# Optimization experiments

Hardware: AMD Instinct MI355X
Metric: run time of the kernel (lower is better)

## Reference

```python
import jax, jax.numpy as jnp
import numpy as np

T = 16384   # sequence length (timesteps)
E = 1024    # embedding_size
H = 1024    # h_size == vocab (logits are the raw LSTM hidden output)


def setup_inputs() -> dict:
    key = jax.random.key(0)
    ks = jax.random.split(key, 6)
    s = 1.0 / np.sqrt(H)  # torch LSTM default init: U(-1/sqrt(H), 1/sqrt(H))
    Xs = jax.random.normal(ks[0], (T, E), jnp.float32)
    W_ih = jax.random.uniform(ks[1], (4 * H, E), jnp.float32, -s, s)
    W_hh = jax.random.uniform(ks[2], (4 * H, H), jnp.float32, -s, s)
    b_ih = jax.random.uniform(ks[3], (4 * H,), jnp.float32, -s, s)
    b_hh = jax.random.uniform(ks[4], (4 * H,), jnp.float32, -s, s)
    ys = jax.random.randint(ks[5], (T,), 0, H, dtype=jnp.int64)
    return {"Xs": Xs, "W_ih": W_ih, "W_hh": W_hh, "b_ih": b_ih, "b_hh": b_hh, "ys": ys}


def reference(Xs, W_ih, W_hh, b_ih, b_hh, ys):
    h_size = W_hh.shape[1]
    # input projections for all timesteps in one GEMM: [T, 4H]
    xg = Xs @ W_ih.T + b_ih + b_hh

    def step(carry, inp):
        h, c = carry
        xg_t, y_t = inp
        gates = xg_t + W_hh @ h  # [4H], torch gate order i,f,g,o
        i = jax.nn.sigmoid(gates[0 * h_size:1 * h_size])
        f = jax.nn.sigmoid(gates[1 * h_size:2 * h_size])
        g = jnp.tanh(gates[2 * h_size:3 * h_size])
        o = jax.nn.sigmoid(gates[3 * h_size:4 * h_size])
        c = f * c + i * g
        h = o * jnp.tanh(c)
        # cross-entropy on raw hidden output (vocab == h_size), batch 1
        loss_t = jax.nn.logsumexp(h) - h[y_t]
        return (h, c), loss_t

    h0 = jnp.zeros((h_size,), Xs.dtype)
    c0 = jnp.zeros((h_size,), Xs.dtype)
    (_, _), losses = jax.lax.scan(step, (h0, c0), (xg, ys))
    return jnp.sum(losses)
```

## Files before the change

kernel.cpp:

```cpp
#include <hip/hip_runtime.h>
#include <hip/hip_cooperative_groups.h>
#include <cstddef>

namespace cg = cooperative_groups;

#define T_STEPS 16384
#define E_DIM   1024
#define H_DIM   1024
#define G4      4096

#define NWG 128
#define NTH 512
#define EPW 8
#define CH  512
#define NCHUNK (T_STEPS / CH)
#define TKc 32

#define LDA(p)    __hip_atomic_load((p), __ATOMIC_RELAXED, __HIP_MEMORY_SCOPE_AGENT)
#define STA(p, v) __hip_atomic_store((p), (v), __ATOMIC_RELAXED, __HIP_MEMORY_SCOPE_AGENT)


__global__ __launch_bounds__(NTH) void lstm_fused_kernel(
    const float* __restrict__ Xs, const float* __restrict__ Wih,
    const float* __restrict__ Whh, const float* __restrict__ bih,
    const float* __restrict__ bhh, const int* __restrict__ ys,
    float* __restrict__ xgc,
    unsigned long long* __restrict__ hslot,
    float* __restrict__ partials,
    float* __restrict__ hy,
    float* __restrict__ wsum,
    float* __restrict__ out)
{
    cg::grid_group grid = cg::this_grid();
    const int w    = blockIdx.x;
    const int tid  = threadIdx.x;
    const int lane = tid & 63;
    const int j    = tid >> 6;
    const int gj   = w * EPW + j;

    __shared__ float hs[2][H_DIM];
    __shared__ float ered[16][EPW];
    __shared__ float red[8];
    __shared__ float As[TKc][68];
    __shared__ float Bs[TKc][132];

    float Wreg[4][16];
#pragma unroll
    for (int g = 0; g < 4; ++g) {
        const float* wr = Whh + (size_t)(g * H_DIM + gj) * H_DIM + lane;
#pragma unroll
        for (int m = 0; m < 16; ++m) Wreg[g][m] = wr[m << 6];
    }

    float c_state = 0.f;
    if (lane == 0) STA(&hslot[gj], 1ull << 32);

    const int nt   = w & 31;
    const int n0   = nt * 128;
    const int tx4  = (tid & 31) * 4;
    const int ty4  = (tid >> 5) * 4;
    const int lrow = tid >> 3;
    const int lkg  = (tid & 7) * 4;

    float4 bias_v;
    {
        const float4 bi = *(const float4*)&bih[n0 + tx4];
        const float4 bh = *(const float4*)&bhh[n0 + tx4];
        bias_v.x = bi.x + bh.x; bias_v.y = bi.y + bh.y;
        bias_v.z = bi.z + bh.z; bias_v.w = bi.w + bh.w;
    }

    const float gate_scale = (lane == 2) ? 2.f : 1.f;
    const float gate_mul   = (lane == 2) ? 2.f : 1.f;
    const float gate_add   = (lane == 2) ? -1.f : 0.f;

    float xv = 0.f;
    int   yt = 0;

    for (int c = 0; c < NCHUNK; ++c) {
        const int t0 = c * CH;

#pragma unroll
        for (int rep = 0; rep < 2; ++rep) {
            const int mt = (w >> 5) + rep * 4;
            float acc[4][4];
#pragma unroll
            for (int i = 0; i < 4; ++i)
#pragma unroll
                for (int jj = 0; jj < 4; ++jj) acc[i][jj] = 0.f;

            const float* Arow = Xs + (size_t)(t0 + mt * 64 + lrow) * E_DIM + lkg;

            for (int kc = 0; kc < E_DIM; kc += TKc) {
                __syncthreads();
                float4 av = *(const float4*)(Arow + kc);
                As[lkg + 0][lrow] = av.x; As[lkg + 1][lrow] = av.y;
                As[lkg + 2][lrow] = av.z; As[lkg + 3][lrow] = av.w;
#pragma unroll
                for (int r2 = 0; r2 < 2; ++r2) {
                    int br = r2 * 64 + lrow;
                    float4 bv = *(const float4*)&Wih[(size_t)(n0 + br) * E_DIM + kc + lkg];
                    Bs[lkg + 0][br] = bv.x; Bs[lkg + 1][br] = bv.y;
                    Bs[lkg + 2][br] = bv.z; Bs[lkg + 3][br] = bv.w;
                }
                __syncthreads();
#pragma unroll
                for (int kk = 0; kk < TKc; ++kk) {
                    float4 a = *(const float4*)&As[kk][ty4];
                    float4 b = *(const float4*)&Bs[kk][tx4];
                    acc[0][0] = fmaf(a.x, b.x, acc[0][0]); acc[0][1] = fmaf(a.x, b.y, acc[0][1]);
                    acc[0][2] = fmaf(a.x, b.z, acc[0][2]); acc[0][3] = fmaf(a.x, b.w, acc[0][3]);
                    acc[1][0] = fmaf(a.y, b.x, acc[1][0]); acc[1][1] = fmaf(a.y, b.y, acc[1][1]);
                    acc[1][2] = fmaf(a.y, b.z, acc[1][2]); acc[1][3] = fmaf(a.y, b.w, acc[1][3]);
                    acc[2][0] = fmaf(a.z, b.x, acc[2][0]); acc[2][1] = fmaf(a.z, b.y, acc[2][1]);
                    acc[2][2] = fmaf(a.z, b.z, acc[2][2]); acc[2][3] = fmaf(a.z, b.w, acc[2][3]);
                    acc[3][0] = fmaf(a.w, b.x, acc[3][0]); acc[3][1] = fmaf(a.w, b.y, acc[3][1]);
                    acc[3][2] = fmaf(a.w, b.z, acc[3][2]); acc[3][3] = fmaf(a.w, b.w, acc[3][3]);
                }
            }
#pragma unroll
            for (int i = 0; i < 4; ++i) {
                int lr = mt * 64 + ty4 + i;
                float4 ov;
                ov.x = acc[i][0] + bias_v.x; ov.y = acc[i][1] + bias_v.y;
                ov.z = acc[i][2] + bias_v.z; ov.w = acc[i][3] + bias_v.w;
                *(float4*)&xgc[(size_t)lr * G4 + n0 + tx4] = ov;
            }
        }
        __threadfence();
        grid.sync();

        if (lane < 4) xv = xgc[lane * H_DIM + gj];

        for (int lt = 0; lt < CH; ++lt) {
            const int t = t0 + lt;
            const int p = t & 1;

            if (lane == 0) yt = ys[t];

            {
                const unsigned htag = (unsigned)(t + 1);
                const unsigned long long* hp =
                    hslot + ((size_t)(t & 3) << 10) + 2 * tid;
                unsigned long long v0, v1;
                do {
                    v0 = LDA(hp);
                    v1 = LDA(hp + 1);
                } while ((unsigned)(v0 >> 32) != htag || (unsigned)(v1 >> 32) != htag);
                hs[p][2 * tid]     = __uint_as_float((unsigned)v0);
                hs[p][2 * tid + 1] = __uint_as_float((unsigned)v1);
            }
            __syncthreads();

            if ((t & 7) == 0 && t >= 8 && j == ((t >> 3) & 7)) {
                const int b = t - 8;
                float e = ered[(b & 15) + (lane >> 3)][lane & 7];
                e += __shfl_xor(e, 1);
                e += __shfl_xor(e, 2);
                e += __shfl_xor(e, 4);
                if ((lane & 7) == 0)
                    partials[(size_t)w * T_STEPS + b + (lane >> 3)] = e;
            }

            float xn = 0.f;
            if (lane < 4 && lt + 1 < CH)
                xn = xgc[(size_t)(lt + 1) * G4 + lane * H_DIM + gj];

            float a0 = 0.f, a1 = 0.f, a2 = 0.f, a3 = 0.f;
#pragma unroll
            for (int m = 0; m < 16; ++m) {
                float hvv = hs[p][lane + (m << 6)];
                a0 = fmaf(Wreg[0][m], hvv, a0);
                a1 = fmaf(Wreg[1][m], hvv, a1);
                a2 = fmaf(Wreg[2][m], hvv, a2);
                a3 = fmaf(Wreg[3][m], hvv, a3);
            }
#pragma unroll
            for (int off = 32; off >= 1; off >>= 1) {
                a0 += __shfl_xor(a0, off);
                a1 += __shfl_xor(a1, off);
                a2 += __shfl_xor(a2, off);
                a3 += __shfl_xor(a3, off);
            }

            float sel = (lane == 1) ? a1 : (lane == 2) ? a2 : (lane == 3) ? a3 : a0;
            float x   = sel + xv;
            float sg  = 1.f / (1.f + __expf(-gate_scale * x));
            float act = fmaf(sg, gate_mul, gate_add);

            float ii = act;
            float ff = __shfl(act, 1);
            float gg = __shfl(act, 2);
            float oo = __shfl(act, 3);
            c_state  = fmaf(ff, c_state, ii * gg);
            float tc = 2.f / (1.f + __expf(-2.f * c_state)) - 1.f;
            float h  = oo * tc;

            if (lane == 0) {
                STA(&hslot[((size_t)((t + 1) & 3) << 10) + gj],
                    ((unsigned long long)(unsigned)(t + 2) << 32) |
                    (unsigned long long)__float_as_uint(h));
                ered[t & 15][j] = __expf(h);
                if (gj == yt) hy[t] = h;
            }
            xv = xn;
        }
    }

    __syncthreads();
    if (j == 0) {
        const int b = T_STEPS - 8;
        float e = ered[(b & 15) + (lane >> 3)][lane & 7];
        e += __shfl_xor(e, 1);
        e += __shfl_xor(e, 2);
        e += __shfl_xor(e, 4);
        if ((lane & 7) == 0)
            partials[(size_t)w * T_STEPS + b + (lane >> 3)] = e;
    }
    __threadfence();
    grid.sync();

    if (w < 32) {
        int t = w * NTH + tid;
        float s = 0.f;
        for (int i = 0; i < NWG; ++i) s += partials[(size_t)i * T_STEPS + t];
        float val = logf(s) - hy[t];
#pragma unroll
        for (int off = 32; off >= 1; off >>= 1) val += __shfl_xor(val, off);
        if (lane == 0) red[tid >> 6] = val;
        __syncthreads();
        if (tid == 0) {
            float s2 = 0.f;
#pragma unroll
            for (int i = 0; i < 8; ++i) s2 += red[i];
            wsum[w] = s2;
        }
    }
    __threadfence();
    grid.sync();
    if (w == 0 && tid == 0) {
        float s = 0.f;
        for (int i = 0; i < 32; ++i) s += wsum[i];
        out[0] = s;
    }
}

extern "C" void kernel_launch(void* const* d_in, const int* in_sizes, int n_in,
                              void* d_out, int out_size, void* d_ws, size_t ws_size,
                              hipStream_t stream)
{
    const float* Xs  = (const float*)d_in[0];
    const float* Wih = (const float*)d_in[1];
    const float* Whh = (const float*)d_in[2];
    const float* bih = (const float*)d_in[3];
    const float* bhh = (const float*)d_in[4];
    const int*   ys  = (const int*)d_in[5];

    float* xgc                = (float*)d_ws;
    unsigned long long* hslot = (unsigned long long*)(xgc + (size_t)CH * G4);
    float* partials           = (float*)(hslot + 4 * H_DIM);
    float* hy                 = partials + (size_t)NWG * T_STEPS;
    float* wsum               = hy + T_STEPS;
    float* out                = (float*)d_out;

    void* args[] = {(void*)&Xs, (void*)&Wih, (void*)&Whh, (void*)&bih, (void*)&bhh,
                    (void*)&ys, (void*)&xgc, (void*)&hslot, (void*)&partials,
                    (void*)&hy, (void*)&wsum, (void*)&out};
    hipLaunchCooperativeKernel((void*)lstm_fused_kernel,
                               dim3(NWG), dim3(NTH), args, 0, stream);
}
```

Baseline: 36.06 ms.

## Split workgroups into dedicated GEMM producers and recurrent consumers with double-buffered xg

The kernel now launches 32 extra workgroups that compute the input-projection GEMM for each chunk into a double-buffered xg workspace. The 128 recurrent workgroups run the LSTM steps and meet the producers through flag counters instead of grid-wide barriers. The aim is to overlap the input GEMM with the serial recurrence, so the recurrence no longer stalls at every chunk boundary for the GEMM and a grid.sync. It needs more co-resident workgroups and a second buffer, relies on acquire/release flag ordering being correct, and halves the chunk size, which doubles the handoff count.

Measured after the change: 30.64 ms. 1.18x faster.

```diff
diff --git a/kernel.cpp b/kernel.cpp
--- a/kernel.cpp
+++ b/kernel.cpp
@@ -9,12 +9,14 @@
 #define H_DIM   1024
 #define G4      4096
 
-#define NWG 128
-#define NTH 512
-#define EPW 8
-#define CH  512
-#define NCHUNK (T_STEPS / CH)
-#define TKc 32
+#define NWG_REC  128
+#define NWG_GEMM 32
+#define NWG      (NWG_REC + NWG_GEMM)
+#define NTH      512
+#define EPW      8
+#define CH       256
+#define NCHUNK   (T_STEPS / CH)
+#define TKc      32
 
 #define LDA(p)    __hip_atomic_load((p), __ATOMIC_RELAXED, __HIP_MEMORY_SCOPE_AGENT)
 #define STA(p, v) __hip_atomic_store((p), (v), __ATOMIC_RELAXED, __HIP_MEMORY_SCOPE_AGENT)
@@ -29,6 +31,7 @@
     float* __restrict__ partials,
     float* __restrict__ hy,
     float* __restrict__ wsum,
+    int*   __restrict__ flags,
     float* __restrict__ out)
 {
     cg::grid_group grid = cg::this_grid();
@@ -36,7 +39,6 @@
     const int tid  = threadIdx.x;
     const int lane = tid & 63;
     const int j    = tid >> 6;
-    const int gj   = w * EPW + j;
 
     __shared__ float hs[2][H_DIM];
     __shared__ float ered[16][EPW];
@@ -44,186 +46,218 @@
     __shared__ float As[TKc][68];
     __shared__ float Bs[TKc][132];
 
-    float Wreg[4][16];
-#pragma unroll
-    for (int g = 0; g < 4; ++g) {
-        const float* wr = Whh + (size_t)(g * H_DIM + gj) * H_DIM + lane;
-#pragma unroll
-        for (int m = 0; m < 16; ++m) Wreg[g][m] = wr[m << 6];
-    }
-
-    float c_state = 0.f;
-    if (lane == 0) STA(&hslot[gj], 1ull << 32);
-
-    const int nt   = w & 31;
-    const int n0   = nt * 128;
-    const int tx4  = (tid & 31) * 4;
-    const int ty4  = (tid >> 5) * 4;
-    const int lrow = tid >> 3;
-    const int lkg  = (tid & 7) * 4;
-
-    float4 bias_v;
-    {
-        const float4 bi = *(const float4*)&bih[n0 + tx4];
-        const float4 bh = *(const float4*)&bhh[n0 + tx4];
-        bias_v.x = bi.x + bh.x; bias_v.y = bi.y + bh.y;
-        bias_v.z = bi.z + bh.z; bias_v.w = bi.w + bh.w;
-    }
-
-    const float gate_scale = (lane == 2) ? 2.f : 1.f;
-    const float gate_mul   = (lane == 2) ? 2.f : 1.f;
-    const float gate_add   = (lane == 2) ? -1.f : 0.f;
-
-    float xv = 0.f;
-    int   yt = 0;
-
-    for (int c = 0; c < NCHUNK; ++c) {
-        const int t0 = c * CH;
-
-#pragma unroll
-        for (int rep = 0; rep < 2; ++rep) {
-            const int mt = (w >> 5) + rep * 4;
-            float acc[4][4];
-#pragma unroll
-            for (int i = 0; i < 4; ++i)
-#pragma unroll
-                for (int jj = 0; jj < 4; ++jj) acc[i][jj] = 0.f;
-
-            const float* Arow = Xs + (size_t)(t0 + mt * 64 + lrow) * E_DIM + lkg;
-
-            for (int kc = 0; kc < E_DIM; kc += TKc) {
+    int* chunk_ready = flags;
+    int* cons_done   = flags + 64;
+
+    if (w == 0 && tid < 128) STA(&flags[tid], 0);
+    grid.sync();
+
+    if (w >= NWG_REC) {
+        const int g    = w - NWG_REC;
+        const int n0   = g * 128;
+        const int tx4  = (tid & 31) * 4;
+        const int ty4  = (tid >> 5) * 4;
+        const int lrow = tid >> 3;
+        const int lkg  = (tid & 7) * 4;
+
+        float4 bias_v;
+        {
+            const float4 bi = *(const float4*)&bih[n0 + tx4];
+            const float4 bh = *(const float4*)&bhh[n0 + tx4];
+            bias_v.x = bi.x + bh.x; bias_v.y = bi.y + bh.y;
+            bias_v.z = bi.z + bh.z; bias_v.w = bi.w + bh.w;
+        }
+
+        for (int c = 0; c < NCHUNK; ++c) {
+            if (c >= 2) {
+                if (tid == 0) while (LDA(&cons_done[c - 2]) < NWG_REC) {}
                 __syncthreads();
-                float4 av = *(const float4*)(Arow + kc);
-                As[lkg + 0][lrow] = av.x; As[lkg + 1][lrow] = av.y;
-                As[lkg + 2][lrow] = av.z; As[lkg + 3][lrow] = av.w;
-#pragma unroll
-                for (int r2 = 0; r2 < 2; ++r2) {
-                    int br = r2 * 64 + lrow;
-                    float4 bv = *(const float4*)&Wih[(size_t)(n0 + br) * E_DIM + kc + lkg];
-                    Bs[lkg + 0][br] = bv.x; Bs[lkg + 1][br] = bv.y;
-                    Bs[lkg + 2][br] = bv.z; Bs[lkg + 3][br] = bv.w;
-                }
-                __syncthreads();
-#pragma unroll
-                for (int kk = 0; kk < TKc; ++kk) {
-                    float4 a = *(const float4*)&As[kk][ty4];
-                    float4 b = *(const float4*)&Bs[kk][tx4];
-                    acc[0][0] = fmaf(a.x, b.x, acc[0][0]); acc[0][1] = fmaf(a.x, b.y, acc[0][1]);
-                    acc[0][2] = fmaf(a.x, b.z, acc[0][2]); acc[0][3] = fmaf(a.x, b.w, acc[0][3]);
-                    acc[1][0] = fmaf(a.y, b.x, acc[1][0]); acc[1][1] = fmaf(a.y, b.y, acc[1][1]);
-                    acc[1][2] = fmaf(a.y, b.z, acc[1][2]); acc[1][3] = fmaf(a.y, b.w, acc[1][3]);
-                    acc[2][0] = fmaf(a.z, b.x, acc[2][0]); acc[2][1] = fmaf(a.z, b.y, acc[2][1]);
-                    acc[2][2] = fmaf(a.z, b.z, acc[2][2]); acc[2][3] = fmaf(a.z, b.w, acc[2][3]);
-                    acc[3][0] = fmaf(a.w, b.x, acc[3][0]); acc[3][1] = fmaf(a.w, b.y, acc[3][1]);
-                    acc[3][2] = fmaf(a.w, b.z, acc[3][2]); acc[3][3] = fmaf(a.w, b.w, acc[3][3]);
-                }
             }
-#pragma unroll
-            for (int i = 0; i < 4; ++i) {
-                int lr = mt * 64 + ty4 + i;
-                float4 ov;
-                ov.x = acc[i][0] + bias_v.x; ov.y = acc[i][1] + bias_v.y;
-                ov.z = acc[i][2] + bias_v.z; ov.w = acc[i][3] + bias_v.w;
-                *(float4*)&xgc[(size_t)lr * G4 + n0 + tx4] = ov;
-            }
-        }
-        __threadfence();
-        grid.sync();
-
-        if (lane < 4) xv = xgc[lane * H_DIM + gj];
-
-        for (int lt = 0; lt < CH; ++lt) {
-            const int t = t0 + lt;
-            const int p = t & 1;
-
-            if (lane == 0) yt = ys[t];
-
-            {
-                const unsigned htag = (unsigned)(t + 1);
-                const unsigned long long* hp =
-                    hslot + ((size_t)(t & 3) << 10) + 2 * tid;
-                unsigned long long v0, v1;
-                do {
-                    v0 = LDA(hp);
-                    v1 = LDA(hp + 1);
-                } while ((unsigned)(v0 >> 32) != htag || (unsigned)(v1 >> 32) != htag);
-                hs[p][2 * tid]     = __uint_as_float((unsigned)v0);
-                hs[p][2 * tid + 1] = __uint_as_float((unsigned)v1);
+            const int t0 = c * CH;
+            float* xg = xgc + (size_t)(c & 1) * ((size_t)CH * G4);
+
+#pragma unroll 1
+            for (int rep = 0; rep < 4; ++rep) {
+                float acc[4][4];
+#pragma unroll
+                for (int i = 0; i < 4; ++i)
+#pragma unroll
+                    for (int jj = 0; jj < 4; ++jj) acc[i][jj] = 0.f;
+
+                const float* Arow = Xs + (size_t)(t0 + rep * 64 + lrow) * E_DIM + lkg;
+
+                for (int kc = 0; kc < E_DIM; kc += TKc) {
+                    __syncthreads();
+                    float4 av = *(const float4*)(Arow + kc);
+                    As[lkg + 0][lrow] = av.x; As[lkg + 1][lrow] = av.y;
+                    As[lkg + 2][lrow] = av.z; As[lkg + 3][lrow] = av.w;
+#pragma unroll
+                    for (int r2 = 0; r2 < 2; ++r2) {
+                        int br = r2 * 64 + lrow;
+                        float4 bv = *(const float4*)&Wih[(size_t)(n0 + br) * E_DIM + kc + lkg];
+                        Bs[lkg + 0][br] = bv.x; Bs[lkg + 1][br] = bv.y;
+                        Bs[lkg + 2][br] = bv.z; Bs[lkg + 3][br] = bv.w;
+                    }
+                    __syncthreads();
+#pragma unroll
+                    for (int kk = 0; kk < TKc; ++kk) {
+                        float4 a = *(const float4*)&As[kk][ty4];
+                        float4 b = *(const float4*)&Bs[kk][tx4];
+                        acc[0][0] = fmaf(a.x, b.x, acc[0][0]); acc[0][1] = fmaf(a.x, b.y, acc[0][1]);
+                        acc[0][2] = fmaf(a.x, b.z, acc[0][2]); acc[0][3] = fmaf(a.x, b.w, acc[0][3]);
+                        acc[1][0] = fmaf(a.y, b.x, acc[1][0]); acc[1][1] = fmaf(a.y, b.y, acc[1][1]);
+                        acc[1][2] = fmaf(a.y, b.z, acc[1][2]); acc[1][3] = fmaf(a.y, b.w, acc[1][3]);
+                        acc[2][0] = fmaf(a.z, b.x, acc[2][0]); acc[2][1] = fmaf(a.z, b.y, acc[2][1]);
+                        acc[2][2] = fmaf(a.z, b.z, acc[2][2]); acc[2][3] = fmaf(a.z, b.w, acc[2][3]);
+                        acc[3][0] = fmaf(a.w, b.x, acc[3][0]); acc[3][1] = fmaf(a.w, b.y, acc[3][1]);
+                        acc[3][2] = fmaf(a.w, b.z, acc[3][2]); acc[3][3] = fmaf(a.w, b.w, acc[3][3]);
+                    }
+                }
+#pragma unroll
+                for (int i = 0; i < 4; ++i) {
+                    int lr = rep * 64 + ty4 + i;
+                    float4 ov;
+                    ov.x = acc[i][0] + bias_v.x; ov.y = acc[i][1] + bias_v.y;
+                    ov.z = acc[i][2] + bias_v.z; ov.w = acc[i][3] + bias_v.w;
+                    *(float4*)&xg[(size_t)lr * G4 + n0 + tx4] = ov;
+                }
             }
             __syncthreads();
-
-            if ((t & 7) == 0 && t >= 8 && j == ((t >> 3) & 7)) {
-                const int b = t - 8;
-                float e = ered[(b & 15) + (lane >> 3)][lane & 7];
-                e += __shfl_xor(e, 1);
-                e += __shfl_xor(e, 2);
-                e += __shfl_xor(e, 4);
-                if ((lane & 7) == 0)
-                    partials[(size_t)w * T_STEPS + b + (lane >> 3)] = e;
+            if (tid == 0)
+                __hip_atomic_fetch_add(&chunk_ready[c], 1,
+                                       __ATOMIC_RELEASE, __HIP_MEMORY_SCOPE_AGENT);
+        }
+    } else {
+        const int gj = w * EPW + j;
+
+        float Wreg[4][16];
+#pragma unroll
+        for (int g = 0; g < 4; ++g) {
+            const float* wr = Whh + (size_t)(g * H_DIM + gj) * H_DIM + lane;
+#pragma unroll
+            for (int m = 0; m < 16; ++m) Wreg[g][m] = wr[m << 6];
+        }
+
+        float c_state = 0.f;
+        if (lane == 0) STA(&hslot[gj], 1ull << 32);
+
+        const float gate_scale = (lane == 2) ? 2.f : 1.f;
+        const float gate_mul   = (lane == 2) ? 2.f : 1.f;
+        const float gate_add   = (lane == 2) ? -1.f : 0.f;
+
+        float xv = 0.f;
+        int   yt = 0;
+
+        for (int c = 0; c < NCHUNK; ++c) {
+            const int t0 = c * CH;
+            const float* xg = xgc + (size_t)(c & 1) * ((size_t)CH * G4);
+
+            if (tid == 0) while (LDA(&chunk_ready[c]) < NWG_GEMM) {}
+            __syncthreads();
+            (void)__hip_atomic_load(&chunk_ready[c],
+                                    __ATOMIC_ACQUIRE, __HIP_MEMORY_SCOPE_AGENT);
+
+            if (lane < 4) xv = xg[lane * H_DIM + gj];
+
+            for (int lt = 0; lt < CH; ++lt) {
+                const int t = t0 + lt;
+                const int p = t & 1;
+
+                if (lane == 0) yt = ys[t];
+
+                {
+                    const unsigned htag = (unsigned)(t + 1);
+                    const unsigned long long* hp =
+                        hslot + ((size_t)(t & 3) << 10) + 2 * tid;
+                    unsigned long long v0, v1;
+                    do {
+                        v0 = LDA(hp);
+                        v1 = LDA(hp + 1);
+                    } while ((unsigned)(v0 >> 32) != htag || (unsigned)(v1 >> 32) != htag);
+                    hs[p][2 * tid]     = __uint_as_float((unsigned)v0);
+                    hs[p][2 * tid + 1] = __uint_as_float((unsigned)v1);
+                }
+                __syncthreads();
+
+                if ((t & 7) == 0 && t >= 8 && j == ((t >> 3) & 7)) {
+                    const int b = t - 8;
+                    float e = ered[(b & 15) + (lane >> 3)][lane & 7];
+                    e += __shfl_xor(e, 1);
+                    e += __shfl_xor(e, 2);
+                    e += __shfl_xor(e, 4);
+                    if ((lane & 7) == 0)
+                        partials[(size_t)w * T_STEPS + b + (lane >> 3)] = e;
+                }
+
+                float xn = 0.f;
+                if (lane < 4 && lt + 1 < CH)
+                    xn = xg[(size_t)(lt + 1) * G4 + lane * H_DIM + gj];
+
+                float a0 = 0.f, a1 = 0.f, a2 = 0.f, a3 = 0.f;
+#pragma unroll
+                for (int m = 0; m < 16; ++m) {
+                    float hvv = hs[p][lane + (m << 6)];
+                    a0 = fmaf(Wreg[0][m], hvv, a0);
+                    a1 = fmaf(Wreg[1][m], hvv, a1);
+                    a2 = fmaf(Wreg[2][m], hvv, a2);
+                    a3 = fmaf(Wreg[3][m], hvv, a3);
+                }
+#pragma unroll
+                for (int off = 32; off >= 1; off >>= 1) {
+                    a0 += __shfl_xor(a0, off);
+                    a1 += __shfl_xor(a1, off);
+                    a2 += __shfl_xor(a2, off);
+                    a3 += __shfl_xor(a3, off);
+                }
+
+                float sel = (lane == 1) ? a1 : (lane == 2) ? a2 : (lane == 3) ? a3 : a0;
+                float x   = sel + xv;
+                float sg  = 1.f / (1.f + __expf(-gate_scale * x));
+                float act = fmaf(sg, gate_mul, gate_add);
+
+                float ii = act;
+                float ff = __shfl(act, 1);
+                float gg = __shfl(act, 2);
+                float oo = __shfl(act, 3);
+                c_state  = fmaf(ff, c_state, ii * gg);
+                float tc = 2.f / (1.f + __expf(-2.f * c_state)) - 1.f;
+                float h  = oo * tc;
+
+                if (lane == 0) {
+                    STA(&hslot[((size_t)((t + 1) & 3) << 10) + gj],
+                        ((unsigned long long)(unsigned)(t + 2) << 32) |
+                        (unsigned long long)__float_as_uint(h));
+                    ered[t & 15][j] = __expf(h);
+                    if (gj == yt) hy[t] = h;
+                }
+                xv = xn;
             }
 
-            float xn = 0.f;
-            if (lane < 4 && lt + 1 < CH)
-                xn = xgc[(size_t)(lt + 1) * G4 + lane * H_DIM + gj];
-
-            float a0 = 0.f, a1 = 0.f, a2 = 0.f, a3 = 0.f;
-#pragma unroll
-            for (int m = 0; m < 16; ++m) {
-                float hvv = hs[p][lane + (m << 6)];
-                a0 = fmaf(Wreg[0][m], hvv, a0);
-                a1 = fmaf(Wreg[1][m], hvv, a1);
-                a2 = fmaf(Wreg[2][m], hvv, a2);
-                a3 = fmaf(Wreg[3][m], hvv, a3);
-            }
-#pragma unroll
-            for (int off = 32; off >= 1; off >>= 1) {
-                a0 += __shfl_xor(a0, off);
-                a1 += __shfl_xor(a1, off);
-                a2 += __shfl_xor(a2, off);
-                a3 += __shfl_xor(a3, off);
-            }
-
-            float sel = (lane == 1) ? a1 : (lane == 2) ? a2 : (lane == 3) ? a3 : a0;
-            float x   = sel + xv;
-            float sg  = 1.f / (1.f + __expf(-gate_scale * x));
-            float act = fmaf(sg, gate_mul, gate_add);
-
-            float ii = act;
-            float ff = __shfl(act, 1);
-            float gg = __shfl(act, 2);
-            float oo = __shfl(act, 3);
-            c_state  = fmaf(ff, c_state, ii * gg);
-            float tc = 2.f / (1.f + __expf(-2.f * c_state)) - 1.f;
-            float h  = oo * tc;
-
-            if (lane == 0) {
-                STA(&hslot[((size_t)((t + 1) & 3) << 10) + gj],
-                    ((unsigned long long)(unsigned)(t + 2) << 32) |
-                    (unsigned long long)__float_as_uint(h));
-                ered[t & 15][j] = __expf(h);
-                if (gj == yt) hy[t] = h;
-            }
-            xv = xn;
+            __syncthreads();
+            if (tid == 0)
+                __hip_atomic_fetch_add(&cons_done[c], 1,
+                                       __ATOMIC_RELAXED, __HIP_MEMORY_SCOPE_AGENT);
+        }
+
+        __syncthreads();
+        if (j == 0) {
+            const int b = T_STEPS - 8;
+            float e = ered[(b & 15) + (lane >> 3)][lane & 7];
+            e += __shfl_xor(e, 1);
+            e += __shfl_xor(e, 2);
+            e += __shfl_xor(e, 4);
+            if ((lane & 7) == 0)
+                partials[(size_t)w * T_STEPS + b + (lane >> 3)] = e;
         }
     }
 
-    __syncthreads();
-    if (j == 0) {
-        const int b = T_STEPS - 8;
-        float e = ered[(b & 15) + (lane >> 3)][lane & 7];
-        e += __shfl_xor(e, 1);
-        e += __shfl_xor(e, 2);
-        e += __shfl_xor(e, 4);
-        if ((lane & 7) == 0)
-            partials[(size_t)w * T_STEPS + b + (lane >> 3)] = e;
-    }
     __threadfence();
     grid.sync();
 
     if (w < 32) {
         int t = w * NTH + tid;
         float s = 0.f;
-        for (int i = 0; i < NWG; ++i) s += partials[(size_t)i * T_STEPS + t];
+        for (int i = 0; i < NWG_REC; ++i) s += partials[(size_t)i * T_STEPS + t];
         float val = logf(s) - hy[t];
 #pragma unroll
         for (int off = 32; off >= 1; off >>= 1) val += __shfl_xor(val, off);
@@ -257,15 +291,16 @@
     const int*   ys  = (const int*)d_in[5];
 
     float* xgc                = (float*)d_ws;
-    unsigned long long* hslot = (unsigned long long*)(xgc + (size_t)CH * G4);
+    unsigned long long* hslot = (unsigned long long*)(xgc + 2 * (size_t)CH * G4);
     float* partials           = (float*)(hslot + 4 * H_DIM);
-    float* hy                 = partials + (size_t)NWG * T_STEPS;
+    float* hy                 = partials + (size_t)NWG_REC * T_STEPS;
     float* wsum               = hy + T_STEPS;
+    int*   flags              = (int*)(wsum + 32);
     float* out                = (float*)d_out;
 
     void* args[] = {(void*)&Xs, (void*)&Wih, (void*)&Whh, (void*)&bih, (void*)&bhh,
                     (void*)&ys, (void*)&xgc, (void*)&hslot, (void*)&partials,
-                    (void*)&hy, (void*)&wsum, (void*)&out};
+                    (void*)&hy, (void*)&wsum, (void*)&flags, (void*)&out};
     hipLaunchCooperativeKernel((void*)lstm_fused_kernel,
                                dim3(NWG), dim3(NTH), args, 0, stream);
 }
```
